# Kernel tuning notes

Hardware: AMD Instinct MI355X
Metric: run time of the kernel (lower is better)

Reference implementation:

```python
import jax, jax.numpy as jnp
import numpy as np

B, NV, L = 64, 8, 1024
P = 16            # patch_len == stride (non-overlapping)
D, H, DFF = 768, 12, 3072
K = D // H        # head dim 64
T = L // P        # 64 patches per sequence
N = B * NV        # 512 flattened sequences


def _ln(x, g, b, eps=1e-5):
    m = x.mean(-1, keepdims=True)
    v = x.var(-1, keepdims=True)
    return (x - m) / jnp.sqrt(v + eps) * g + b


def _pos_emb():
    pos = jnp.arange(T, dtype=jnp.float32)[:, None]
    div = jnp.exp(jnp.arange(0, D, 2, dtype=jnp.float32) * (-np.log(10000.0) / D))
    pe = jnp.zeros((T, D), jnp.float32)
    pe = pe.at[:, 0::2].set(jnp.sin(pos * div))
    pe = pe.at[:, 1::2].set(jnp.cos(pos * div))
    return pe


def setup_inputs() -> dict:
    key = jax.random.key(0)
    ks = jax.random.split(key, 24)
    rn = lambda k, s: jax.random.normal(k, s, jnp.float32) * 0.02
    return dict(
        x=jax.random.normal(ks[0], (B, NV, L), jnp.float32),
        W_patch=rn(ks[1], (P, D)), b_patch=jnp.zeros((D,), jnp.float32),
        ln1_g=jnp.ones((D,), jnp.float32), ln1_b=jnp.zeros((D,), jnp.float32),
        ln2_g=jnp.ones((D,), jnp.float32), ln2_b=jnp.zeros((D,), jnp.float32),
        mu_r=jax.random.uniform(ks[2], (D,), jnp.float32),
        mu_w=jax.random.uniform(ks[3], (D,), jnp.float32),
        mu_k=jax.random.uniform(ks[4], (D,), jnp.float32),
        mu_v=jax.random.uniform(ks[5], (D,), jnp.float32),
        mu_a=jax.random.uniform(ks[6], (D,), jnp.float32),
        mu_g=jax.random.uniform(ks[7], (D,), jnp.float32),
        mu_c=jax.random.uniform(ks[8], (D,), jnp.float32),
        Wr=rn(ks[9], (D, D)), Wk=rn(ks[10], (D, D)), Wv=rn(ks[11], (D, D)),
        Wg=rn(ks[12], (D, D)), Ww=rn(ks[13], (D, D)), w0=rn(ks[14], (D,)),
        Wa=rn(ks[15], (D, D)), a0=jnp.zeros((D,), jnp.float32),
        Wo=rn(ks[16], (D, D)),
        gn_g=jnp.ones((D,), jnp.float32), gn_b=jnp.zeros((D,), jnp.float32),
        Wc1=rn(ks[17], (D, DFF)), Wc2=rn(ks[18], (DFF, D)),
        W_proj=rn(ks[19], (D, P)), b_proj=jnp.zeros((P,), jnp.float32),
    )


def reference(x, W_patch, b_patch, ln1_g, ln1_b, ln2_g, ln2_b,
              mu_r, mu_w, mu_k, mu_v, mu_a, mu_g, mu_c,
              Wr, Wk, Wv, Wg, Ww, w0, Wa, a0, Wo, gn_g, gn_b,
              Wc1, Wc2, W_proj, b_proj):
    # --- patch embedding (stride == patch_len -> plain reshape) ---
    patches = x.reshape(B, NV, T, P).reshape(N, T, P)
    h = patches @ W_patch + b_patch + _pos_emb()        # [N, T, D]

    # --- RWKV7 time mixing ---
    xx = _ln(h, ln1_g, ln1_b)
    sh = jnp.pad(xx[:, :-1], ((0, 0), (1, 0), (0, 0)))  # token shift
    lerp = lambda mu: xx + (sh - xx) * mu
    r = (lerp(mu_r) @ Wr).reshape(N, T, H, K)
    k = (lerp(mu_k) @ Wk).reshape(N, T, H, K)
    v = (lerp(mu_v) @ Wv).reshape(N, T, H, K)
    w = jnp.exp(-jnp.exp(lerp(mu_w) @ Ww + w0)).reshape(N, T, H, K)  # decay in (0,1)
    a = jax.nn.sigmoid(lerp(mu_a) @ Wa + a0).reshape(N, T, H, K)     # in-context lr
    g = jax.nn.sigmoid(lerp(mu_g) @ Wg)                              # output gate [N,T,D]
    kk = k / (jnp.linalg.norm(k, axis=-1, keepdims=True) + 1e-6)     # removal key

    seq = tuple(jnp.transpose(t, (1, 0, 2, 3)) for t in (r, w, k, v, kk, a))

    def step(S, inp):
        # S: [N, H, V, K] value-by-key state (generalized delta rule)
        r_t, w_t, k_t, v_t, kk_t, a_t = inp
        S = S * w_t[:, :, None, :]
        sa = jnp.einsum('nhvk,nhk->nhv', S, kk_t)
        S = S - jnp.einsum('nhv,nhk->nhvk', sa, kk_t * a_t) \
              + jnp.einsum('nhv,nhk->nhvk', v_t, k_t)
        y = jnp.einsum('nhvk,nhk->nhv', S, r_t)
        return S, y

    S0 = jnp.zeros((N, H, K, K), x.dtype)
    _, ys = jax.lax.scan(step, S0, seq)
    y = jnp.transpose(ys, (1, 0, 2, 3))                 # [N, T, H, K]

    # per-head group norm (RWKV7 uses eps = 64e-5)
    m = y.mean(-1, keepdims=True)
    var = y.var(-1, keepdims=True)
    y = (y - m) / jnp.sqrt(var + 64e-5)
    y = y.reshape(N, T, D) * gn_g + gn_b
    h = h + (y * g) @ Wo

    # --- channel mixing (squared-ReLU FFN) ---
    xc = _ln(h, ln2_g, ln2_b)
    shc = jnp.pad(xc[:, :-1], ((0, 0), (1, 0), (0, 0)))
    xk = xc + (shc - xc) * mu_c
    h = h + jnp.square(jax.nn.relu(xk @ Wc1)) @ Wc2

    # --- projection back to patch space ---
    return h @ W_proj + b_proj                          # [N, T, P]
```

## Files before the change

kernel.cpp:

```cpp
#include <hip/hip_runtime.h>
#include <hip/hip_bf16.h>
#include <math.h>

typedef unsigned short u16;
typedef unsigned int u32;
typedef _Float16 f16x8 __attribute__((ext_vector_type(8)));
typedef float f32x4 __attribute__((ext_vector_type(4)));

#define DEV static __device__ __forceinline__

constexpr int D = 768;
constexpr int HH = 12;
constexpr int KD = 64;
constexpr int T = 64;
constexpr int NSEQ = 512;
constexpr int MROWS = NSEQ * T;
constexpr int DFF = 3072;
constexpr int PP = 16;

DEV u16 f2h(float f){ union{_Float16 h; u16 u;} c; c.h = (_Float16)f; return c.u; }
DEV float h2f(u16 u){ union{u16 u; _Float16 h;} c; c.u = u; return (float)c.h; }
DEV void gld_lds16(const u16* g, u16* l){
  __builtin_amdgcn_global_load_lds((const __attribute__((address_space(1))) void*)g,
                                   (__attribute__((address_space(3))) void*)l, 16, 0, 0);
}

struct TpArgs { const float* src[7]; u16* dst[7]; };
__global__ __launch_bounds__(256) void k_transpose7(TpArgs a){
  __shared__ float tile[32][33];
  int z = blockIdx.z;
  const float* W = a.src[z];
  u16* WT = a.dst[z];
  int c0 = blockIdx.x * 32, r0 = blockIdx.y * 32;
  int tx = threadIdx.x, ty = threadIdx.y;
  #pragma unroll
  for (int i = 0; i < 32; i += 8)
    tile[ty + i][tx] = W[(size_t)(r0 + ty + i) * D + (c0 + tx)];
  __syncthreads();
  #pragma unroll
  for (int i = 0; i < 32; i += 8)
    WT[(size_t)(c0 + ty + i) * D + (r0 + tx)] = f2h(tile[tx][ty + i]);
}

__global__ __launch_bounds__(256) void k_transpose(const float* __restrict__ W, u16* __restrict__ WT,
                                                   int R, int C){
  __shared__ float tile[32][33];
  int c0 = blockIdx.x * 32, r0 = blockIdx.y * 32;
  int tx = threadIdx.x, ty = threadIdx.y;
  #pragma unroll
  for (int i = 0; i < 32; i += 8)
    tile[ty + i][tx] = W[(size_t)(r0 + ty + i) * C + (c0 + tx)];
  __syncthreads();
  #pragma unroll
  for (int i = 0; i < 32; i += 8)
    WT[(size_t)(c0 + ty + i) * R + (r0 + tx)] = f2h(tile[tx][ty + i]);
}

__global__ void k_pe(float* __restrict__ pe){
  int idx = blockIdx.x * 256 + threadIdx.x;
  if (idx >= T * D) return;
  int t = idx / D, d = idx % D;
  float dv = __expf((float)(d & ~1) * (-9.210340371976184f / (float)D));
  float ang = (float)t * dv;
  pe[idx] = (d & 1) ? cosf(ang) : sinf(ang);
}

struct PrepArgs { const float* mu[6]; };
__global__ __launch_bounds__(256) void k_patchmix(const float* __restrict__ x, const float* __restrict__ Wp,
                                                  const float* __restrict__ bp, const float* __restrict__ pe,
                                                  const float* __restrict__ g, const float* __restrict__ b,
                                                  PrepArgs pa, float* __restrict__ h,
                                                  u16* __restrict__ planes, size_t psz){
  int lane = threadIdx.x & 63;
  int row = blockIdx.x * 4 + (threadIdx.x >> 6);
  int t = row & (T - 1);
  const float* xr = x + (size_t)row * PP;
  float xs[PP];
  #pragma unroll
  for (int p = 0; p < PP; p++) xs[p] = xr[p];
  float v[12], s = 0.f, sq = 0.f;
  #pragma unroll
  for (int j = 0; j < 12; j++){
    int d = lane + j * 64;
    float acc = bp[d] + pe[t * D + d];
    #pragma unroll
    for (int p = 0; p < PP; p++) acc = fmaf(xs[p], Wp[p * D + d], acc);
    v[j] = acc; s += acc; sq = fmaf(acc, acc, sq);
  }
  #pragma unroll
  for (int o = 32; o; o >>= 1){ s += __shfl_xor(s, o); sq += __shfl_xor(sq, o); }
  float mean = s * (1.f / 768.f);
  float rstd = rsqrtf(sq * (1.f / 768.f) - mean * mean + 1e-5f);
  float p12[12], meanp = 0.f, rstdp = 0.f;
  if (t){
    const float* xq = xr - PP;
    float xsp[PP];
    #pragma unroll
    for (int p = 0; p < PP; p++) xsp[p] = xq[p];
    float sp = 0.f, sqp = 0.f;
    #pragma unroll
    for (int j = 0; j < 12; j++){
      int d = lane + j * 64;
      float acc = bp[d] + pe[(t - 1) * D + d];
      #pragma unroll
      for (int p = 0; p < PP; p++) acc = fmaf(xsp[p], Wp[p * D + d], acc);
      p12[j] = acc; sp += acc; sqp = fmaf(acc, acc, sqp);
    }
    #pragma unroll
    for (int o = 32; o; o >>= 1){ sp += __shfl_xor(sp, o); sqp += __shfl_xor(sqp, o); }
    meanp = sp * (1.f / 768.f);
    rstdp = rsqrtf(sqp * (1.f / 768.f) - meanp * meanp + 1e-5f);
  }
  float* hrow = h + (size_t)row * D;
  size_t rofs = (size_t)row * D;
  #pragma unroll
  for (int j = 0; j < 12; j++){
    int d = lane + j * 64;
    hrow[d] = v[j];
    float cm = (v[j] - mean) * rstd * g[d] + b[d];
    float cp = t ? (p12[j] - meanp) * rstdp * g[d] + b[d] : 0.f;
    float dd = cp - cm;
    #pragma unroll
    for (int z = 0; z < 6; z++)
      planes[z * psz + rofs + d] = f2h(cm + dd * pa.mu[z][d]);
  }
}

__global__ __launch_bounds__(256) void k_ln2(const float* __restrict__ X, const float* __restrict__ g,
                                             const float* __restrict__ b, const float* __restrict__ mu,
                                             u16* __restrict__ out){
  int lane = threadIdx.x & 63;
  int row = blockIdx.x * 4 + (threadIdx.x >> 6);
  int t = row & (T - 1);
  const float* xr = X + (size_t)row * D;
  float v[12], s = 0.f, sq = 0.f;
  #pragma unroll
  for (int j = 0; j < 12; j++){ v[j] = xr[lane + j * 64]; s += v[j]; sq += v[j] * v[j]; }
  #pragma unroll
  for (int o = 32; o; o >>= 1){ s += __shfl_xor(s, o); sq += __shfl_xor(sq, o); }
  float mean = s * (1.f / 768.f);
  float rstd = rsqrtf(sq * (1.f / 768.f) - mean * mean + 1e-5f);
  float p[12], meanp = 0.f, rstdp = 0.f;
  if (t){
    const float* xp = xr - D;
    float sp = 0.f, sqp = 0.f;
    #pragma unroll
    for (int j = 0; j < 12; j++){ p[j] = xp[lane + j * 64]; sp += p[j]; sqp += p[j] * p[j]; }
    #pragma unroll
    for (int o = 32; o; o >>= 1){ sp += __shfl_xor(sp, o); sqp += __shfl_xor(sqp, o); }
    meanp = sp * (1.f / 768.f);
    rstdp = rsqrtf(sqp * (1.f / 768.f) - meanp * meanp + 1e-5f);
  }
  u16* orow = out + (size_t)row * D;
  #pragma unroll
  for (int j = 0; j < 12; j++){
    int d = lane + j * 64;
    float cm = (v[j] - mean) * rstd * g[d] + b[d];
    float cp = t ? (p[j] - meanp) * rstdp * g[d] + b[d] : 0.f;
    orow[d] = f2h(cm + (cp - cm) * mu[d]);
  }
}

template<int ACT>
__global__ __launch_bounds__(256) void k_g16(const u16* __restrict__ A, const u16* __restrict__ BT,
                                             u16* __restrict__ outH, float* __restrict__ outF,
                                             int Kd, int Nc){
  __shared__ __align__(16) u16 As[128 * 32];
  __shared__ __align__(16) u16 Bs[128 * 32];
  int tid = threadIdx.x;
  int m0 = blockIdx.x * 128, n0 = blockIdx.y * 128;
  int wv = tid >> 6, lane = tid & 63;
  int wr = (wv >> 1) * 64, wc = (wv & 1) * 64;
  int lr = lane & 15, kg = (lane >> 4) * 8;
  int r0 = wv * 16 + (lane >> 2), cb = (lane & 3) * 8;
  const u16* sA0 = A + (size_t)(m0 + r0) * Kd + cb;
  const u16* sA1 = A + (size_t)(m0 + r0 + 64) * Kd + cb;
  const u16* sB0 = BT + (size_t)(n0 + r0) * Kd + cb;
  const u16* sB1 = BT + (size_t)(n0 + r0 + 64) * Kd + cb;
  u16* dA0 = As + r0 * 32 + cb;
  u16* dA1 = As + (r0 + 64) * 32 + cb;
  u16* dB0 = Bs + r0 * 32 + cb;
  u16* dB1 = Bs + (r0 + 64) * 32 + cb;
  f32x4 acc[4][4] = {};

  for (int k0 = 0; k0 < Kd; k0 += 32){
    __syncthreads();
    gld_lds16(sA0 + k0, dA0);
    gld_lds16(sA1 + k0, dA1);
    gld_lds16(sB0 + k0, dB0);
    gld_lds16(sB1 + k0, dB1);
    __syncthreads();
    f16x8 af[4], bf[4];
    #pragma unroll
    for (int mi = 0; mi < 4; mi++) af[mi] = *(const f16x8*)&As[(wr + mi * 16 + lr) * 32 + kg];
    #pragma unroll
    for (int ni = 0; ni < 4; ni++) bf[ni] = *(const f16x8*)&Bs[(wc + ni * 16 + lr) * 32 + kg];
    #pragma unroll
    for (int mi = 0; mi < 4; mi++){
      #pragma unroll
      for (int ni = 0; ni < 4; ni++){
        acc[mi][ni] = __builtin_amdgcn_mfma_f32_16x16x32_f16(af[mi], bf[ni], acc[mi][ni], 0, 0, 0);
      }
    }
  }

  int rowb = m0 + wr + (lane >> 4) * 4;
  int colb = n0 + wc + lr;
  #pragma unroll
  for (int mi = 0; mi < 4; mi++){
    #pragma unroll
    for (int ni = 0; ni < 4; ni++){
      int gcol = colb + ni * 16;
      #pragma unroll
      for (int i = 0; i < 4; i++){
        int grow = rowb + mi * 16 + i;
        float xv = acc[mi][ni][i];
        size_t o = (size_t)grow * Nc + gcol;
        if (ACT == 3){ float rl = fmaxf(xv, 0.f); outH[o] = f2h(rl * rl); }
        else outF[o] += xv;
      }
    }
  }
}

struct MixArgs {
  const u16* a[6]; const u16* b[6]; const float* bias[6];
  u16* outh[6]; float* outf[6]; int act[6];
};
__global__ __launch_bounds__(256) void k_mix(MixArgs args, int Kd, int Nc){
  __shared__ __align__(16) u16 As[128 * 32];
  __shared__ __align__(16) u16 Bs[128 * 32];
  int tid = threadIdx.x, z = blockIdx.z;
  const u16* A = args.a[z];
  const u16* BT = args.b[z];
  int m0 = blockIdx.x * 128, n0 = blockIdx.y * 128;
  int wv = tid >> 6, lane = tid & 63;
  int wr = (wv >> 1) * 64, wc = (wv & 1) * 64;
  int lr = lane & 15, kg = (lane >> 4) * 8;
  int r0 = wv * 16 + (lane >> 2), cb = (lane & 3) * 8;
  const u16* sA0 = A + (size_t)(m0 + r0) * Kd + cb;
  const u16* sA1 = A + (size_t)(m0 + r0 + 64) * Kd + cb;
  const u16* sB0 = BT + (size_t)(n0 + r0) * Kd + cb;
  const u16* sB1 = BT + (size_t)(n0 + r0 + 64) * Kd + cb;
  u16* dA0 = As + r0 * 32 + cb;
  u16* dA1 = As + (r0 + 64) * 32 + cb;
  u16* dB0 = Bs + r0 * 32 + cb;
  u16* dB1 = Bs + (r0 + 64) * 32 + cb;
  f32x4 acc[4][4] = {};

  for (int k0 = 0; k0 < Kd; k0 += 32){
    __syncthreads();
    gld_lds16(sA0 + k0, dA0);
    gld_lds16(sA1 + k0, dA1);
    gld_lds16(sB0 + k0, dB0);
    gld_lds16(sB1 + k0, dB1);
    __syncthreads();
    f16x8 af[4], bf[4];
    #pragma unroll
    for (int mi = 0; mi < 4; mi++) af[mi] = *(const f16x8*)&As[(wr + mi * 16 + lr) * 32 + kg];
    #pragma unroll
    for (int ni = 0; ni < 4; ni++) bf[ni] = *(const f16x8*)&Bs[(wc + ni * 16 + lr) * 32 + kg];
    #pragma unroll
    for (int mi = 0; mi < 4; mi++){
      #pragma unroll
      for (int ni = 0; ni < 4; ni++){
        acc[mi][ni] = __builtin_amdgcn_mfma_f32_16x16x32_f16(af[mi], bf[ni], acc[mi][ni], 0, 0, 0);
      }
    }
  }

  int act = args.act[z];
  const float* bias = args.bias[z];
  u16* outh = args.outh[z];
  float* outf = args.outf[z];
  int rowb = m0 + wr + (lane >> 4) * 4;
  int colb = n0 + wc + lr;
  #pragma unroll
  for (int mi = 0; mi < 4; mi++){
    #pragma unroll
    for (int ni = 0; ni < 4; ni++){
      int gcol = colb + ni * 16;
      float bv = bias ? bias[gcol] : 0.f;
      #pragma unroll
      for (int i = 0; i < 4; i++){
        int grow = rowb + mi * 16 + i;
        float xv = acc[mi][ni][i] + bv;
        size_t o = (size_t)grow * Nc + gcol;
        if (act == 0)      outh[o] = f2h(xv);
        else if (act == 1) outf[o] = __expf(-__expf(xv));
        else               outh[o] = f2h(1.f / (1.f + __expf(-xv)));
      }
    }
  }
}

constexpr int TS = 8;
__global__ __launch_bounds__(256) void k_rwkv(const u16* __restrict__ rb16, const float* __restrict__ wf,
                                              const u16* __restrict__ kb16, const u16* __restrict__ vb,
                                              const u16* __restrict__ ab, const u16* __restrict__ gbuf,
                                              const float* __restrict__ gng, const float* __restrict__ gnb,
                                              u16* __restrict__ yg){
  __shared__ __align__(16) float ls_w[TS][64], ls_k[TS][64], ls_r[TS][64];
  __shared__ float ls_v[TS][64], ls_a[TS][64];
  __shared__ float ls_kk[TS][64], ls_ka[TS][64];
  __shared__ float sa_red[2][4][64];
  __shared__ float y_red[2][4][64];
  int nh = blockIdx.x;
  int n = nh / HH, hh = nh - n * HH;
  int tid = threadIdx.x;
  int wv = __builtin_amdgcn_readfirstlane(tid >> 6);
  int lane = tid & 63;
  float S[16];
  #pragma unroll
  for (int i = 0; i < 16; i++) S[i] = 0.f;
  int dcol = hh * KD + lane;
  float gscale = gng[dcol], gshift = gnb[dcol];
  size_t hbase = (size_t)n * T * D + hh * KD;
  int jbase = wv * 16;
  int strow = tid >> 5;
  int stcol = (tid & 31) * 2;
  for (int tt = 0; tt < T; tt += TS){
    __syncthreads();
    size_t gofs = hbase + (size_t)(tt + strow) * D + stcol;
    *(float2*)&ls_w[strow][stcol] = *(const float2*)(wf + gofs);
    u32 k2 = *(const u32*)(kb16 + gofs);
    u32 r2 = *(const u32*)(rb16 + gofs);
    u32 v2 = *(const u32*)(vb + gofs);
    u32 a2 = *(const u32*)(ab + gofs);
    ls_k[strow][stcol]     = h2f((u16)(k2 & 0xffffu));
    ls_k[strow][stcol + 1] = h2f((u16)(k2 >> 16));
    ls_r[strow][stcol]     = h2f((u16)(r2 & 0xffffu));
    ls_r[strow][stcol + 1] = h2f((u16)(r2 >> 16));
    ls_v[strow][stcol]     = h2f((u16)(v2 & 0xffffu));
    ls_v[strow][stcol + 1] = h2f((u16)(v2 >> 16));
    ls_a[strow][stcol]     = h2f((u16)(a2 & 0xffffu));
    ls_a[strow][stcol + 1] = h2f((u16)(a2 >> 16));
    __syncthreads();
    #pragma unroll
    for (int rr = 0; rr < 2; rr++){
      int row = wv * 2 + rr;
      float kv = ls_k[row][lane];
      float ss = kv * kv;
      #pragma unroll
      for (int o = 32; o; o >>= 1) ss += __shfl_xor(ss, o);
      float kk = kv / (sqrtf(ss) + 1e-6f);
      ls_kk[row][lane] = kk;
      ls_ka[row][lane] = kk * ls_a[row][lane];
    }
    __syncthreads();
    for (int s = 0; s < TS; s++){
      int sg = tt + s;
      int pb = sg & 1;
      f32x4 W4[4], KK4[4];
      #pragma unroll
      for (int q = 0; q < 4; q++){
        W4[q]  = *(const f32x4*)&ls_w[s][jbase + q * 4];
        KK4[q] = *(const f32x4*)&ls_kk[s][jbase + q * 4];
      }
      float sap = 0.f;
      #pragma unroll
      for (int q = 0; q < 4; q++){
        #pragma unroll
        for (int i = 0; i < 4; i++){
          S[q * 4 + i] *= W4[q][i];
          sap += S[q * 4 + i] * KK4[q][i];
        }
      }
      sa_red[pb][wv][lane] = sap;
      __syncthreads();
      if (wv == 0 && sg > 0){
        int pp = pb ^ 1;
        float y = y_red[pp][0][lane] + y_red[pp][1][lane] + y_red[pp][2][lane] + y_red[pp][3][lane];
        float s1 = y, s2 = y * y;
        #pragma unroll
        for (int o = 32; o; o >>= 1){ s1 += __shfl_xor(s1, o); s2 += __shfl_xor(s2, o); }
        float mean = s1 * (1.f / 64.f);
        float var = s2 * (1.f / 64.f) - mean * mean;
        float yn = (y - mean) * rsqrtf(var + 64e-5f);
        size_t pidx = hbase + (size_t)(sg - 1) * D + lane;
        float gv = h2f(gbuf[pidx]);
        yg[pidx] = f2h((yn * gscale + gshift) * gv);
      }
      float sa = sa_red[pb][0][lane] + sa_red[pb][1][lane] + sa_red[pb][2][lane] + sa_red[pb][3][lane];
      float nsa = -sa;
      float vl = ls_v[s][lane];
      f32x4 K4[4], KA4[4], R4[4];
      #pragma unroll
      for (int q = 0; q < 4; q++){
        K4[q]  = *(const f32x4*)&ls_k[s][jbase + q * 4];
        KA4[q] = *(const f32x4*)&ls_ka[s][jbase + q * 4];
        R4[q]  = *(const f32x4*)&ls_r[s][jbase + q * 4];
      }
      float yp = 0.f;
      #pragma unroll
      for (int q = 0; q < 4; q++){
        #pragma unroll
        for (int i = 0; i < 4; i++){
          S[q * 4 + i] = fmaf(vl, K4[q][i], S[q * 4 + i]);
          S[q * 4 + i] = fmaf(nsa, KA4[q][i], S[q * 4 + i]);
          yp += S[q * 4 + i] * R4[q][i];
        }
      }
      y_red[pb][wv][lane] = yp;
    }
  }
  __syncthreads();
  if (wv == 0){
    int pp = (T - 1) & 1;
    float y = y_red[pp][0][lane] + y_red[pp][1][lane] + y_red[pp][2][lane] + y_red[pp][3][lane];
    float s1 = y, s2 = y * y;
    #pragma unroll
    for (int o = 32; o; o >>= 1){ s1 += __shfl_xor(s1, o); s2 += __shfl_xor(s2, o); }
    float mean = s1 * (1.f / 64.f);
    float var = s2 * (1.f / 64.f) - mean * mean;
    float yn = (y - mean) * rsqrtf(var + 64e-5f);
    size_t pidx = hbase + (size_t)(T - 1) * D + lane;
    float gv = h2f(gbuf[pidx]);
    yg[pidx] = f2h((yn * gscale + gshift) * gv);
  }
}

__global__ __launch_bounds__(256) void k_proj(const float* __restrict__ Hb, const float* __restrict__ Wp,
                                              const float* __restrict__ bp, float* __restrict__ out){
  int lane = threadIdx.x & 63;
  int row = blockIdx.x * 4 + (threadIdx.x >> 6);
  int p = lane & 15, q = lane >> 4;
  const float* hr = Hb + (size_t)row * D;
  float acc = 0.f;
  #pragma unroll 8
  for (int i = 0; i < 192; i++){
    int d = q * 192 + i;
    acc = fmaf(hr[d], Wp[d * PP + p], acc);
  }
  acc += __shfl_xor(acc, 16);
  acc += __shfl_xor(acc, 32);
  if (q == 0) out[(size_t)row * PP + p] = acc + bp[p];
}

extern "C" void kernel_launch(void* const* d_in, const int* in_sizes, int n_in,
                              void* d_out, int out_size, void* d_ws, size_t ws_size,
                              hipStream_t stream){
  (void)in_sizes; (void)n_in; (void)out_size;
  const float* x       = (const float*)d_in[0];
  const float* W_patch = (const float*)d_in[1];
  const float* b_patch = (const float*)d_in[2];
  const float* ln1_g   = (const float*)d_in[3];
  const float* ln1_b   = (const float*)d_in[4];
  const float* ln2_g   = (const float*)d_in[5];
  const float* ln2_b   = (const float*)d_in[6];
  const float* mu_r    = (const float*)d_in[7];
  const float* mu_w    = (const float*)d_in[8];
  const float* mu_k    = (const float*)d_in[9];
  const float* mu_v    = (const float*)d_in[10];
  const float* mu_a    = (const float*)d_in[11];
  const float* mu_g    = (const float*)d_in[12];
  const float* mu_c    = (const float*)d_in[13];
  const float* Wr      = (const float*)d_in[14];
  const float* Wk      = (const float*)d_in[15];
  const float* Wv      = (const float*)d_in[16];
  const float* Wg      = (const float*)d_in[17];
  const float* Ww      = (const float*)d_in[18];
  const float* w0      = (const float*)d_in[19];
  const float* Wa      = (const float*)d_in[20];
  const float* a0      = (const float*)d_in[21];
  const float* Wo      = (const float*)d_in[22];
  const float* gn_g    = (const float*)d_in[23];
  const float* gn_b    = (const float*)d_in[24];
  const float* Wc1     = (const float*)d_in[25];
  const float* Wc2     = (const float*)d_in[26];
  const float* W_proj  = (const float*)d_in[27];
  const float* b_proj  = (const float*)d_in[28];
  float* out = (float*)d_out;

  char* ws = (char*)d_ws;
  size_t off = 0;
  auto alloc = [&](size_t bytes) -> char* {
    char* p = ws + off;
    off = (off + bytes + 255) & ~(size_t)255;
    return p;
  };

  const size_t WB = (size_t)D * D * 2;
  u16* WrT  = (u16*)alloc(WB);
  u16* WwT  = (u16*)alloc(WB);
  u16* WkT  = (u16*)alloc(WB);
  u16* WvT  = (u16*)alloc(WB);
  u16* WaT  = (u16*)alloc(WB);
  u16* WgT  = (u16*)alloc(WB);
  u16* WoT  = (u16*)alloc(WB);
  u16* Wc1T = (u16*)alloc((size_t)D * DFF * 2);
  u16* Wc2T = (u16*)alloc((size_t)DFF * D * 2);
  float* pe = (float*)alloc((size_t)T * D * 4);
  size_t wend = off;

  int nch = 1;
  size_t Mc = MROWS;
  while (nch < 128){
    size_t need = wend + Mc * 23040 + 64 * 256;
    if (need <= ws_size) break;
    nch *= 2;
    Mc >>= 1;
  }
  float* hbuf = (float*)alloc(Mc * 768 * 4);
  u16* ap     = (u16*)alloc(6 * Mc * 768 * 2);
  float* wf   = (float*)alloc(Mc * 768 * 4);
  u16* rb     = (u16*)alloc(Mc * 768 * 2);
  u16* kb     = (u16*)alloc(Mc * 768 * 2);
  u16* vb     = (u16*)alloc(Mc * 768 * 2);
  u16* ab     = (u16*)alloc(Mc * 768 * 2);
  u16* gb     = (u16*)alloc(Mc * 768 * 2);
  u16* ygb    = ab;
  u16* mid    = ap;
  u16* xkb    = kb;

  dim3 tb(32, 8);
  TpArgs ta;
  ta.src[0] = Wr; ta.dst[0] = WrT;
  ta.src[1] = Ww; ta.dst[1] = WwT;
  ta.src[2] = Wk; ta.dst[2] = WkT;
  ta.src[3] = Wv; ta.dst[3] = WvT;
  ta.src[4] = Wa; ta.dst[4] = WaT;
  ta.src[5] = Wg; ta.dst[5] = WgT;
  ta.src[6] = Wo; ta.dst[6] = WoT;
  k_transpose7<<<dim3(24, 24, 7), tb, 0, stream>>>(ta);
  k_transpose<<<dim3(96, 24), tb, 0, stream>>>(Wc1, Wc1T, D, DFF);
  k_transpose<<<dim3(24, 96), tb, 0, stream>>>(Wc2, Wc2T, DFF, D);
  k_pe<<<dim3(192), dim3(256), 0, stream>>>(pe);

  PrepArgs pmu;
  pmu.mu[0] = mu_r; pmu.mu[1] = mu_w; pmu.mu[2] = mu_k;
  pmu.mu[3] = mu_v; pmu.mu[4] = mu_a; pmu.mu[5] = mu_g;

  MixArgs margs;
  const u16* wts[6] = {WrT, WwT, WkT, WvT, WaT, WgT};
  const float* bss[6] = {nullptr, w0, nullptr, nullptr, a0, nullptr};
  u16* oh[6] = {rb, nullptr, kb, vb, ab, gb};
  float* of[6] = {nullptr, wf, nullptr, nullptr, nullptr, nullptr};
  int acts[6] = {0, 1, 0, 0, 2, 2};
  for (int z = 0; z < 6; z++){
    margs.a[z] = ap + (size_t)z * Mc * 768;
    margs.b[z] = wts[z];
    margs.bias[z] = bss[z];
    margs.outh[z] = oh[z];
    margs.outf[z] = of[z];
    margs.act[z] = acts[z];
  }

  for (int c = 0; c < nch; ++c){
    const float* xc = x + (size_t)c * Mc * PP;
    float* outc = out + (size_t)c * Mc * PP;
    int mcb = (int)(Mc / 128);

    k_patchmix<<<dim3((int)(Mc / 4)), dim3(256), 0, stream>>>(xc, W_patch, b_patch, pe, ln1_g, ln1_b,
                                                              pmu, hbuf, ap, Mc * 768);

    k_mix<<<dim3(mcb, 6, 6), 256, 0, stream>>>(margs, D, D);

    k_rwkv<<<dim3((int)(Mc / T) * HH), dim3(256), 0, stream>>>(rb, wf, kb, vb, ab, gb, gn_g, gn_b, ygb);

    k_g16<4><<<dim3(mcb, 6), 256, 0, stream>>>(ygb, WoT, nullptr, hbuf, D, D);

    k_ln2<<<dim3((int)(Mc / 4)), dim3(256), 0, stream>>>(hbuf, ln2_g, ln2_b, mu_c, xkb);
    k_g16<3><<<dim3(mcb, DFF / 128), 256, 0, stream>>>(xkb, Wc1T, mid, nullptr, D, DFF);
    k_g16<4><<<dim3(mcb, 6), 256, 0, stream>>>(mid, Wc2T, nullptr, hbuf, DFF, D);

    k_proj<<<dim3((int)(Mc / 4)), dim3(256), 0, stream>>>(hbuf, W_proj, b_proj, outc);
  }
}
```

Before: 1.954 ms.

## Fuse token-shift lerp into mixing GEMM A-tile load to shrink workspace

```diff
diff --git a/kernel.cpp b/kernel.cpp
--- a/kernel.cpp
+++ b/kernel.cpp
@@ -5,6 +5,7 @@
 typedef unsigned short u16;
 typedef unsigned int u32;
 typedef _Float16 f16x8 __attribute__((ext_vector_type(8)));
+typedef short s16x4 __attribute__((ext_vector_type(4)));
 typedef float f32x4 __attribute__((ext_vector_type(4)));
 
 #define DEV static __device__ __forceinline__
@@ -66,6 +67,41 @@
 }
 
 struct PrepArgs { const float* mu[6]; };
+
+__global__ __launch_bounds__(256) void k_patch_ln(const float* __restrict__ x, const float* __restrict__ Wp,
+                                                  const float* __restrict__ bp, const float* __restrict__ pe,
+                                                  const float* __restrict__ g, const float* __restrict__ b,
+                                                  float* __restrict__ h, float* __restrict__ xxf){
+  int lane = threadIdx.x & 63;
+  int row = blockIdx.x * 4 + (threadIdx.x >> 6);
+  int t = row & (T - 1);
+  const float* xr = x + (size_t)row * PP;
+  float xs[PP];
+  #pragma unroll
+  for (int p = 0; p < PP; p++) xs[p] = xr[p];
+  float v[12], s = 0.f, sq = 0.f;
+  #pragma unroll
+  for (int j = 0; j < 12; j++){
+    int d = lane + j * 64;
+    float acc = bp[d] + pe[t * D + d];
+    #pragma unroll
+    for (int p = 0; p < PP; p++) acc = fmaf(xs[p], Wp[p * D + d], acc);
+    v[j] = acc; s += acc; sq = fmaf(acc, acc, sq);
+  }
+  #pragma unroll
+  for (int o = 32; o; o >>= 1){ s += __shfl_xor(s, o); sq += __shfl_xor(sq, o); }
+  float mean = s * (1.f / 768.f);
+  float rstd = rsqrtf(sq * (1.f / 768.f) - mean * mean + 1e-5f);
+  float* hrow = h + (size_t)row * D;
+  float* xrow = xxf + (size_t)row * D;
+  #pragma unroll
+  for (int j = 0; j < 12; j++){
+    int d = lane + j * 64;
+    hrow[d] = v[j];
+    xrow[d] = (v[j] - mean) * rstd * g[d] + b[d];
+  }
+}
+
 __global__ __launch_bounds__(256) void k_patchmix(const float* __restrict__ x, const float* __restrict__ Wp,
                                                   const float* __restrict__ bp, const float* __restrict__ pe,
                                                   const float* __restrict__ g, const float* __restrict__ b,
@@ -224,9 +260,10 @@
 }
 
 struct MixArgs {
-  const u16* a[6]; const u16* b[6]; const float* bias[6];
+  const u16* a[6]; const u16* b[6]; const float* bias[6]; const float* mu[6];
   u16* outh[6]; float* outf[6]; int act[6];
 };
+
 __global__ __launch_bounds__(256) void k_mix(MixArgs args, int Kd, int Nc){
   __shared__ __align__(16) u16 As[128 * 32];
   __shared__ __align__(16) u16 Bs[128 * 32];
@@ -254,6 +291,85 @@
     gld_lds16(sA1 + k0, dA1);
     gld_lds16(sB0 + k0, dB0);
     gld_lds16(sB1 + k0, dB1);
+    __syncthreads();
+    f16x8 af[4], bf[4];
+    #pragma unroll
+    for (int mi = 0; mi < 4; mi++) af[mi] = *(const f16x8*)&As[(wr + mi * 16 + lr) * 32 + kg];
+    #pragma unroll
+    for (int ni = 0; ni < 4; ni++) bf[ni] = *(const f16x8*)&Bs[(wc + ni * 16 + lr) * 32 + kg];
+    #pragma unroll
+    for (int mi = 0; mi < 4; mi++){
+      #pragma unroll
+      for (int ni = 0; ni < 4; ni++){
+        acc[mi][ni] = __builtin_amdgcn_mfma_f32_16x16x32_f16(af[mi], bf[ni], acc[mi][ni], 0, 0, 0);
+      }
+    }
+  }
+
+  int act = args.act[z];
+  const float* bias = args.bias[z];
+  u16* outh = args.outh[z];
+  float* outf = args.outf[z];
+  int rowb = m0 + wr + (lane >> 4) * 4;
+  int colb = n0 + wc + lr;
+  #pragma unroll
+  for (int mi = 0; mi < 4; mi++){
+    #pragma unroll
+    for (int ni = 0; ni < 4; ni++){
+      int gcol = colb + ni * 16;
+      float bv = bias ? bias[gcol] : 0.f;
+      #pragma unroll
+      for (int i = 0; i < 4; i++){
+        int grow = rowb + mi * 16 + i;
+        float xv = acc[mi][ni][i] + bv;
+        size_t o = (size_t)grow * Nc + gcol;
+        if (act == 0)      outh[o] = f2h(xv);
+        else if (act == 1) outf[o] = __expf(-__expf(xv));
+        else               outh[o] = f2h(1.f / (1.f + __expf(-xv)));
+      }
+    }
+  }
+}
+
+__global__ __launch_bounds__(256) void k_mix_lerp(const float* __restrict__ X, MixArgs args, int Kd, int Nc){
+  __shared__ __align__(16) u16 As[128 * 32];
+  __shared__ __align__(16) u16 Bs[128 * 32];
+  int tid = threadIdx.x, z = blockIdx.z;
+  const u16* BT = args.b[z];
+  const float* mu = args.mu[z];
+  int m0 = blockIdx.x * 128, n0 = blockIdx.y * 128;
+  int wv = tid >> 6, lane = tid & 63;
+  int wr = (wv >> 1) * 64, wc = (wv & 1) * 64;
+  int lr = lane & 15, kg = (lane >> 4) * 8;
+  int r0 = wv * 16 + (lane >> 2), cb = (lane & 3) * 8;
+  const u16* sB0 = BT + (size_t)(n0 + r0) * Kd + cb;
+  const u16* sB1 = BT + (size_t)(n0 + r0 + 64) * Kd + cb;
+  u16* dB0 = Bs + r0 * 32 + cb;
+  u16* dB1 = Bs + (r0 + 64) * 32 + cb;
+  f32x4 acc[4][4] = {};
+
+  for (int k0 = 0; k0 < Kd; k0 += 32){
+    __syncthreads();
+    gld_lds16(sB0 + k0, dB0);
+    gld_lds16(sB1 + k0, dB1);
+    #pragma unroll
+    for (int pass = 0; pass < 4; pass++){
+      int c = pass * 256 + tid;
+      int rr = c >> 3, c4 = (c & 7) * 4;
+      int row = m0 + rr;
+      bool tnz = (row & (T - 1)) != 0;
+      const float* src = X + (size_t)row * Kd + k0 + c4;
+      float4 cur = *(const float4*)src;
+      float4 prv = tnz ? *(const float4*)(src - Kd) : make_float4(0.f, 0.f, 0.f, 0.f);
+      float* cf = (float*)&cur; float* pf = (float*)&prv;
+      s16x4 pk;
+      #pragma unroll
+      for (int j = 0; j < 4; j++){
+        float m = mu[k0 + c4 + j];
+        pk[j] = (short)f2h(cf[j] + (pf[j] - cf[j]) * m);
+      }
+      *(s16x4*)&As[rr * 32 + c4] = pk;
+    }
     __syncthreads();
     f16x8 af[4], bf[4];
     #pragma unroll
@@ -493,25 +609,13 @@
   float* pe = (float*)alloc((size_t)T * D * 4);
   size_t wend = off;
 
-  int nch = 1;
-  size_t Mc = MROWS;
-  while (nch < 128){
-    size_t need = wend + Mc * 23040 + 64 * 256;
-    if (need <= ws_size) break;
-    nch *= 2;
-    Mc >>= 1;
-  }
-  float* hbuf = (float*)alloc(Mc * 768 * 4);
-  u16* ap     = (u16*)alloc(6 * Mc * 768 * 2);
-  float* wf   = (float*)alloc(Mc * 768 * 4);
-  u16* rb     = (u16*)alloc(Mc * 768 * 2);
-  u16* kb     = (u16*)alloc(Mc * 768 * 2);
-  u16* vb     = (u16*)alloc(Mc * 768 * 2);
-  u16* ab     = (u16*)alloc(Mc * 768 * 2);
-  u16* gb     = (u16*)alloc(Mc * 768 * 2);
-  u16* ygb    = ab;
-  u16* mid    = ap;
-  u16* xkb    = kb;
+  size_t McF = MROWS; int nchF = 1;
+  while (nchF < 128 && wend + McF * 16896 + 16384 > ws_size){ nchF *= 2; McF >>= 1; }
+  size_t McA = MROWS; int nchA = 1;
+  while (nchA < 128 && wend + McA * 23040 + 16384 > ws_size){ nchA *= 2; McA >>= 1; }
+  bool fused = McF > McA;
+  size_t Mc = fused ? McF : McA;
+  int nch = fused ? nchF : nchA;
 
   dim3 tb(32, 8);
   TpArgs ta;
@@ -531,39 +635,90 @@
   pmu.mu[0] = mu_r; pmu.mu[1] = mu_w; pmu.mu[2] = mu_k;
   pmu.mu[3] = mu_v; pmu.mu[4] = mu_a; pmu.mu[5] = mu_g;
 
-  MixArgs margs;
   const u16* wts[6] = {WrT, WwT, WkT, WvT, WaT, WgT};
   const float* bss[6] = {nullptr, w0, nullptr, nullptr, a0, nullptr};
-  u16* oh[6] = {rb, nullptr, kb, vb, ab, gb};
-  float* of[6] = {nullptr, wf, nullptr, nullptr, nullptr, nullptr};
   int acts[6] = {0, 1, 0, 0, 2, 2};
-  for (int z = 0; z < 6; z++){
-    margs.a[z] = ap + (size_t)z * Mc * 768;
-    margs.b[z] = wts[z];
-    margs.bias[z] = bss[z];
-    margs.outh[z] = oh[z];
-    margs.outf[z] = of[z];
-    margs.act[z] = acts[z];
-  }
-
-  for (int c = 0; c < nch; ++c){
-    const float* xc = x + (size_t)c * Mc * PP;
-    float* outc = out + (size_t)c * Mc * PP;
-    int mcb = (int)(Mc / 128);
-
-    k_patchmix<<<dim3((int)(Mc / 4)), dim3(256), 0, stream>>>(xc, W_patch, b_patch, pe, ln1_g, ln1_b,
-                                                              pmu, hbuf, ap, Mc * 768);
-
-    k_mix<<<dim3(mcb, 6, 6), 256, 0, stream>>>(margs, D, D);
-
-    k_rwkv<<<dim3((int)(Mc / T) * HH), dim3(256), 0, stream>>>(rb, wf, kb, vb, ab, gb, gn_g, gn_b, ygb);
-
-    k_g16<4><<<dim3(mcb, 6), 256, 0, stream>>>(ygb, WoT, nullptr, hbuf, D, D);
-
-    k_ln2<<<dim3((int)(Mc / 4)), dim3(256), 0, stream>>>(hbuf, ln2_g, ln2_b, mu_c, xkb);
-    k_g16<3><<<dim3(mcb, DFF / 128), 256, 0, stream>>>(xkb, Wc1T, mid, nullptr, D, DFF);
-    k_g16<4><<<dim3(mcb, 6), 256, 0, stream>>>(mid, Wc2T, nullptr, hbuf, DFF, D);
-
-    k_proj<<<dim3((int)(Mc / 4)), dim3(256), 0, stream>>>(hbuf, W_proj, b_proj, outc);
-  }
-}
+
+  if (fused){
+    float* hbuf = (float*)alloc(Mc * 768 * 4);
+    float* xxf  = (float*)alloc(Mc * 768 * 4);
+    float* wf   = (float*)alloc(Mc * 768 * 4);
+    u16* rb     = (u16*)alloc(Mc * 768 * 2);
+    u16* kb     = (u16*)alloc(Mc * 768 * 2);
+    u16* vb     = (u16*)alloc(Mc * 768 * 2);
+    u16* ab     = (u16*)alloc(Mc * 768 * 2);
+    u16* gb     = (u16*)alloc(Mc * 768 * 2);
+    u16* ygb = ab;
+    u16* mid = (u16*)xxf;
+    u16* xkb = kb;
+
+    MixArgs margs;
+    u16* oh[6] = {rb, nullptr, kb, vb, ab, gb};
+    float* of[6] = {nullptr, wf, nullptr, nullptr, nullptr, nullptr};
+    for (int z = 0; z < 6; z++){
+      margs.a[z] = nullptr;
+      margs.b[z] = wts[z];
+      margs.bias[z] = bss[z];
+      margs.mu[z] = pmu.mu[z];
+      margs.outh[z] = oh[z];
+      margs.outf[z] = of[z];
+      margs.act[z] = acts[z];
+    }
+
+    for (int c = 0; c < nch; ++c){
+      const float* xc = x + (size_t)c * Mc * PP;
+      float* outc = out + (size_t)c * Mc * PP;
+      int mcb = (int)(Mc / 128);
+
+      k_patch_ln<<<dim3((int)(Mc / 4)), dim3(256), 0, stream>>>(xc, W_patch, b_patch, pe, ln1_g, ln1_b, hbuf, xxf);
+      k_mix_lerp<<<dim3(mcb, 6, 6), 256, 0, stream>>>(xxf, margs, D, D);
+      k_rwkv<<<dim3((int)(Mc / T) * HH), dim3(256), 0, stream>>>(rb, wf, kb, vb, ab, gb, gn_g, gn_b, ygb);
+      k_g16<4><<<dim3(mcb, 6), 256, 0, stream>>>(ygb, WoT, nullptr, hbuf, D, D);
+      k_ln2<<<dim3((int)(Mc / 4)), dim3(256), 0, stream>>>(hbuf, ln2_g, ln2_b, mu_c, xkb);
+      k_g16<3><<<dim3(mcb, DFF / 128), 256, 0, stream>>>(xkb, Wc1T, mid, nullptr, D, DFF);
+      k_g16<4><<<dim3(mcb, 6), 256, 0, stream>>>(mid, Wc2T, nullptr, hbuf, DFF, D);
+      k_proj<<<dim3((int)(Mc / 4)), dim3(256), 0, stream>>>(hbuf, W_proj, b_proj, outc);
+    }
+  } else {
+    float* hbuf = (float*)alloc(Mc * 768 * 4);
+    u16* ap     = (u16*)alloc(6 * Mc * 768 * 2);
+    float* wf   = (float*)alloc(Mc * 768 * 4);
+    u16* rb     = (u16*)alloc(Mc * 768 * 2);
+    u16* kb     = (u16*)alloc(Mc * 768 * 2);
+    u16* vb     = (u16*)alloc(Mc * 768 * 2);
+    u16* ab     = (u16*)alloc(Mc * 768 * 2);
+    u16* gb     = (u16*)alloc(Mc * 768 * 2);
+    u16* ygb = ab;
+    u16* mid = ap;
+    u16* xkb = kb;
+
+    MixArgs margs;
+    u16* oh[6] = {rb, nullptr, kb, vb, ab, gb};
+    float* of[6] = {nullptr, wf, nullptr, nullptr, nullptr, nullptr};
+    for (int z = 0; z < 6; z++){
+      margs.a[z] = ap + (size_t)z * Mc * 768;
+      margs.b[z] = wts[z];
+      margs.bias[z] = bss[z];
+      margs.mu[z] = pmu.mu[z];
+      margs.outh[z] = oh[z];
+      margs.outf[z] = of[z];
+      margs.act[z] = acts[z];
+    }
+
+    for (int c = 0; c < nch; ++c){
+      const float* xc = x + (size_t)c * Mc * PP;
+      float* outc = out + (size_t)c * Mc * PP;
+      int mcb = (int)(Mc / 128);
+
+      k_patchmix<<<dim3((int)(Mc / 4)), dim3(256), 0, stream>>>(xc, W_patch, b_patch, pe, ln1_g, ln1_b,
+                                                                pmu, hbuf, ap, Mc * 768);
+      k_mix<<<dim3(mcb, 6, 6), 256, 0, stream>>>(margs, D, D);
+      k_rwkv<<<dim3((int)(Mc / T) * HH), dim3(256), 0, stream>>>(rb, wf, kb, vb, ab, gb, gn_g, gn_b, ygb);
+      k_g16<4><<<dim3(mcb, 6), 256, 0, stream>>>(ygb, WoT, nullptr, hbuf, D, D);
+      k_ln2<<<dim3((int)(Mc / 4)), dim3(256), 0, stream>>>(hbuf, ln2_g, ln2_b, mu_c, xkb);
+      k_g16<3><<<dim3(mcb, DFF / 128), 256, 0, stream>>>(xkb, Wc1T, mid, nullptr, D, DFF);
+      k_g16<4><<<dim3(mcb, 6), 256, 0, stream>>>(mid, Wc2T, nullptr, hbuf, DFF, D);
+      k_proj<<<dim3((int)(Mc / 4)), dim3(256), 0, stream>>>(hbuf, W_proj, b_proj, outc);
+    }
+  }
+}
```

After: 1.960 ms. No clear change (+0.3%).

## Fuse token-shift lerp into mix GEMM A-load and store w pre-activation in fp16

Applied to the files above, without the earlier changes.

```diff
diff --git a/kernel.cpp b/kernel.cpp
--- a/kernel.cpp
+++ b/kernel.cpp
@@ -65,12 +65,10 @@
   pe[idx] = (d & 1) ? cosf(ang) : sinf(ang);
 }
 
-struct PrepArgs { const float* mu[6]; };
-__global__ __launch_bounds__(256) void k_patchmix(const float* __restrict__ x, const float* __restrict__ Wp,
+__global__ __launch_bounds__(256) void k_patch_ln(const float* __restrict__ x, const float* __restrict__ Wp,
                                                   const float* __restrict__ bp, const float* __restrict__ pe,
                                                   const float* __restrict__ g, const float* __restrict__ b,
-                                                  PrepArgs pa, float* __restrict__ h,
-                                                  u16* __restrict__ planes, size_t psz){
+                                                  float* __restrict__ h, u16* __restrict__ xx16){
   int lane = threadIdx.x & 63;
   int row = blockIdx.x * 4 + (threadIdx.x >> 6);
   int t = row & (T - 1);
@@ -91,38 +89,13 @@
   for (int o = 32; o; o >>= 1){ s += __shfl_xor(s, o); sq += __shfl_xor(sq, o); }
   float mean = s * (1.f / 768.f);
   float rstd = rsqrtf(sq * (1.f / 768.f) - mean * mean + 1e-5f);
-  float p12[12], meanp = 0.f, rstdp = 0.f;
-  if (t){
-    const float* xq = xr - PP;
-    float xsp[PP];
-    #pragma unroll
-    for (int p = 0; p < PP; p++) xsp[p] = xq[p];
-    float sp = 0.f, sqp = 0.f;
-    #pragma unroll
-    for (int j = 0; j < 12; j++){
-      int d = lane + j * 64;
-      float acc = bp[d] + pe[(t - 1) * D + d];
-      #pragma unroll
-      for (int p = 0; p < PP; p++) acc = fmaf(xsp[p], Wp[p * D + d], acc);
-      p12[j] = acc; sp += acc; sqp = fmaf(acc, acc, sqp);
-    }
-    #pragma unroll
-    for (int o = 32; o; o >>= 1){ sp += __shfl_xor(sp, o); sqp += __shfl_xor(sqp, o); }
-    meanp = sp * (1.f / 768.f);
-    rstdp = rsqrtf(sqp * (1.f / 768.f) - meanp * meanp + 1e-5f);
-  }
   float* hrow = h + (size_t)row * D;
-  size_t rofs = (size_t)row * D;
+  u16* xrow = xx16 + (size_t)row * D;
   #pragma unroll
   for (int j = 0; j < 12; j++){
     int d = lane + j * 64;
     hrow[d] = v[j];
-    float cm = (v[j] - mean) * rstd * g[d] + b[d];
-    float cp = t ? (p12[j] - meanp) * rstdp * g[d] + b[d] : 0.f;
-    float dd = cp - cm;
-    #pragma unroll
-    for (int z = 0; z < 6; z++)
-      planes[z * psz + rofs + d] = f2h(cm + dd * pa.mu[z][d]);
+    xrow[d] = f2h((v[j] - mean) * rstd * g[d] + b[d]);
   }
 }
 
@@ -224,36 +197,52 @@
 }
 
 struct MixArgs {
-  const u16* a[6]; const u16* b[6]; const float* bias[6];
-  u16* outh[6]; float* outf[6]; int act[6];
+  const u16* b[6]; const float* bias[6]; const float* mu[6];
+  u16* outh[6]; int act[6];
 };
-__global__ __launch_bounds__(256) void k_mix(MixArgs args, int Kd, int Nc){
+__global__ __launch_bounds__(256) void k_mix_lerp(const u16* __restrict__ X16, MixArgs args, int Kd, int Nc){
   __shared__ __align__(16) u16 As[128 * 32];
   __shared__ __align__(16) u16 Bs[128 * 32];
   int tid = threadIdx.x, z = blockIdx.z;
-  const u16* A = args.a[z];
   const u16* BT = args.b[z];
+  const float* mu = args.mu[z];
   int m0 = blockIdx.x * 128, n0 = blockIdx.y * 128;
   int wv = tid >> 6, lane = tid & 63;
   int wr = (wv >> 1) * 64, wc = (wv & 1) * 64;
   int lr = lane & 15, kg = (lane >> 4) * 8;
   int r0 = wv * 16 + (lane >> 2), cb = (lane & 3) * 8;
-  const u16* sA0 = A + (size_t)(m0 + r0) * Kd + cb;
-  const u16* sA1 = A + (size_t)(m0 + r0 + 64) * Kd + cb;
   const u16* sB0 = BT + (size_t)(n0 + r0) * Kd + cb;
   const u16* sB1 = BT + (size_t)(n0 + r0 + 64) * Kd + cb;
-  u16* dA0 = As + r0 * 32 + cb;
-  u16* dA1 = As + (r0 + 64) * 32 + cb;
   u16* dB0 = Bs + r0 * 32 + cb;
   u16* dB1 = Bs + (r0 + 64) * 32 + cb;
   f32x4 acc[4][4] = {};
 
   for (int k0 = 0; k0 < Kd; k0 += 32){
     __syncthreads();
-    gld_lds16(sA0 + k0, dA0);
-    gld_lds16(sA1 + k0, dA1);
     gld_lds16(sB0 + k0, dB0);
     gld_lds16(sB1 + k0, dB1);
+    #pragma unroll
+    for (int pass = 0; pass < 2; pass++){
+      int c = pass * 256 + tid;
+      int rr = c >> 2, c8 = (c & 3) * 8;
+      int row = m0 + rr;
+      bool tnz = (row & (T - 1)) != 0;
+      const u16* src = X16 + (size_t)row * Kd + k0 + c8;
+      uint4 cur = *(const uint4*)src;
+      uint4 prv = tnz ? *(const uint4*)(src - Kd) : make_uint4(0u, 0u, 0u, 0u);
+      const u16* cu = (const u16*)&cur;
+      const u16* pu = (const u16*)&prv;
+      uint4 res;
+      u16* ru = (u16*)&res;
+      #pragma unroll
+      for (int j = 0; j < 8; j++){
+        float cf = h2f(cu[j]);
+        float pf = tnz ? h2f(pu[j]) : 0.f;
+        float m = mu[k0 + c8 + j];
+        ru[j] = f2h(cf + (pf - cf) * m);
+      }
+      *(uint4*)&As[rr * 32 + c8] = res;
+    }
     __syncthreads();
     f16x8 af[4], bf[4];
     #pragma unroll
@@ -272,7 +261,6 @@
   int act = args.act[z];
   const float* bias = args.bias[z];
   u16* outh = args.outh[z];
-  float* outf = args.outf[z];
   int rowb = m0 + wr + (lane >> 4) * 4;
   int colb = n0 + wc + lr;
   #pragma unroll
@@ -286,16 +274,15 @@
         int grow = rowb + mi * 16 + i;
         float xv = acc[mi][ni][i] + bv;
         size_t o = (size_t)grow * Nc + gcol;
-        if (act == 0)      outh[o] = f2h(xv);
-        else if (act == 1) outf[o] = __expf(-__expf(xv));
-        else               outh[o] = f2h(1.f / (1.f + __expf(-xv)));
+        if (act == 2) xv = 1.f / (1.f + __expf(-xv));
+        outh[o] = f2h(xv);
       }
     }
   }
 }
 
 constexpr int TS = 8;
-__global__ __launch_bounds__(256) void k_rwkv(const u16* __restrict__ rb16, const float* __restrict__ wf,
+__global__ __launch_bounds__(256) void k_rwkv(const u16* __restrict__ rb16, const u16* __restrict__ wp16,
                                               const u16* __restrict__ kb16, const u16* __restrict__ vb,
                                               const u16* __restrict__ ab, const u16* __restrict__ gbuf,
                                               const float* __restrict__ gng, const float* __restrict__ gnb,
@@ -322,11 +309,13 @@
   for (int tt = 0; tt < T; tt += TS){
     __syncthreads();
     size_t gofs = hbase + (size_t)(tt + strow) * D + stcol;
-    *(float2*)&ls_w[strow][stcol] = *(const float2*)(wf + gofs);
+    u32 w2 = *(const u32*)(wp16 + gofs);
     u32 k2 = *(const u32*)(kb16 + gofs);
     u32 r2 = *(const u32*)(rb16 + gofs);
     u32 v2 = *(const u32*)(vb + gofs);
     u32 a2 = *(const u32*)(ab + gofs);
+    ls_w[strow][stcol]     = __expf(-__expf(h2f((u16)(w2 & 0xffffu))));
+    ls_w[strow][stcol + 1] = __expf(-__expf(h2f((u16)(w2 >> 16))));
     ls_k[strow][stcol]     = h2f((u16)(k2 & 0xffffu));
     ls_k[strow][stcol + 1] = h2f((u16)(k2 >> 16));
     ls_r[strow][stcol]     = h2f((u16)(r2 & 0xffffu));
@@ -496,22 +485,22 @@
   int nch = 1;
   size_t Mc = MROWS;
   while (nch < 128){
-    size_t need = wend + Mc * 23040 + 64 * 256;
+    size_t need = wend + Mc * 13824 + 64 * 256;
     if (need <= ws_size) break;
     nch *= 2;
     Mc >>= 1;
   }
   float* hbuf = (float*)alloc(Mc * 768 * 4);
-  u16* ap     = (u16*)alloc(6 * Mc * 768 * 2);
-  float* wf   = (float*)alloc(Mc * 768 * 4);
+  u16* xx     = (u16*)alloc(Mc * 768 * 2);
+  u16* wp     = (u16*)alloc(Mc * 768 * 2);
   u16* rb     = (u16*)alloc(Mc * 768 * 2);
   u16* kb     = (u16*)alloc(Mc * 768 * 2);
   u16* vb     = (u16*)alloc(Mc * 768 * 2);
   u16* ab     = (u16*)alloc(Mc * 768 * 2);
   u16* gb     = (u16*)alloc(Mc * 768 * 2);
-  u16* ygb    = ab;
-  u16* mid    = ap;
-  u16* xkb    = kb;
+  u16* ygb = ab;
+  u16* mid = xx;
+  u16* xkb = gb;
 
   dim3 tb(32, 8);
   TpArgs ta;
@@ -527,22 +516,17 @@
   k_transpose<<<dim3(24, 96), tb, 0, stream>>>(Wc2, Wc2T, DFF, D);
   k_pe<<<dim3(192), dim3(256), 0, stream>>>(pe);
 
-  PrepArgs pmu;
-  pmu.mu[0] = mu_r; pmu.mu[1] = mu_w; pmu.mu[2] = mu_k;
-  pmu.mu[3] = mu_v; pmu.mu[4] = mu_a; pmu.mu[5] = mu_g;
-
   MixArgs margs;
   const u16* wts[6] = {WrT, WwT, WkT, WvT, WaT, WgT};
   const float* bss[6] = {nullptr, w0, nullptr, nullptr, a0, nullptr};
-  u16* oh[6] = {rb, nullptr, kb, vb, ab, gb};
-  float* of[6] = {nullptr, wf, nullptr, nullptr, nullptr, nullptr};
+  const float* mus[6] = {mu_r, mu_w, mu_k, mu_v, mu_a, mu_g};
+  u16* oh[6] = {rb, wp, kb, vb, ab, gb};
   int acts[6] = {0, 1, 0, 0, 2, 2};
   for (int z = 0; z < 6; z++){
-    margs.a[z] = ap + (size_t)z * Mc * 768;
     margs.b[z] = wts[z];
     margs.bias[z] = bss[z];
+    margs.mu[z] = mus[z];
     margs.outh[z] = oh[z];
-    margs.outf[z] = of[z];
     margs.act[z] = acts[z];
   }
 
@@ -551,12 +535,11 @@
     float* outc = out + (size_t)c * Mc * PP;
     int mcb = (int)(Mc / 128);
 
-    k_patchmix<<<dim3((int)(Mc / 4)), dim3(256), 0, stream>>>(xc, W_patch, b_patch, pe, ln1_g, ln1_b,
-                                                              pmu, hbuf, ap, Mc * 768);
-
-    k_mix<<<dim3(mcb, 6, 6), 256, 0, stream>>>(margs, D, D);
-
-    k_rwkv<<<dim3((int)(Mc / T) * HH), dim3(256), 0, stream>>>(rb, wf, kb, vb, ab, gb, gn_g, gn_b, ygb);
+    k_patch_ln<<<dim3((int)(Mc / 4)), dim3(256), 0, stream>>>(xc, W_patch, b_patch, pe, ln1_g, ln1_b, hbuf, xx);
+
+    k_mix_lerp<<<dim3(mcb, 6, 6), 256, 0, stream>>>(xx, margs, D, D);
+
+    k_rwkv<<<dim3((int)(Mc / T) * HH), dim3(256), 0, stream>>>(rb, wp, kb, vb, ab, gb, gn_g, gn_b, ygb);
 
     k_g16<4><<<dim3(mcb, 6), 256, 0, stream>>>(ygb, WoT, nullptr, hbuf, D, D);
 
```

Result: faster. 1.757 ms (-10.1%).
